# Kernel optimization log

Measured on AMD Instinct MI355X. Metric: run time of the kernel, lower is better.

The kernel has to match this reference:

```python
import jax, jax.numpy as jnp
import numpy as np
import math

B, S, D, DH, R = 2, 2048, 1024, 64, 2


def _hex_grid(radius):
    coords = []
    for q in range(-radius, radius + 1):
        for r in range(max(-radius, -q - radius), min(radius, -q + radius) + 1):
            coords.append((q, r))
    return coords


def _adjacency(coords):
    idx = {c: i for i, c in enumerate(coords)}
    H = len(coords)
    A = np.zeros((H, H), dtype=np.float32)
    dirs = [(1, 0), (1, -1), (0, -1), (-1, 0), (-1, 1), (0, 1)]
    for (q, r), i in idx.items():
        for dq, dr in dirs:
            j = idx.get((q + dq, r + dr))
            if j is not None:
                A[i, j] = 1.0
    return A


def setup_inputs() -> dict:
    key = jax.random.key(0)
    ks = jax.random.split(key, 10)
    coords_list = _hex_grid(R)
    H = len(coords_list)  # 19 heads for radius 2
    coords = jnp.asarray(np.array(coords_list, dtype=np.float32))  # [H,2]
    A = _adjacency(coords_list) + np.eye(H, dtype=np.float32)      # self-loops
    adj_norm = jnp.asarray(A / A.sum(axis=1, keepdims=True))       # row-normalized [H,H]
    sd = 1.0 / math.sqrt(D)
    return {
        "x": jax.random.normal(ks[0], (B, S, D), jnp.float32),
        "coords": coords,
        "w_q": jax.random.normal(ks[1], (H, D, DH), jnp.float32) * sd,
        "w_k": jax.random.normal(ks[2], (H, D, DH), jnp.float32) * sd,
        "w_v": jax.random.normal(ks[3], (H, D, DH), jnp.float32) * sd,
        "wb1": jax.random.normal(ks[4], (2, D), jnp.float32) * 0.5,
        "bb1": jnp.zeros((D,), jnp.float32),
        "wb2": jax.random.normal(ks[5], (D, DH), jnp.float32) * sd,
        "bb2": jnp.zeros((DH,), jnp.float32),
        "w_mix": jax.random.normal(ks[6], (DH, DH), jnp.float32) / math.sqrt(DH),
        "adj_norm": adj_norm,
        "w_o": jax.random.normal(ks[7], (H * DH, D), jnp.float32) * sd,
    }


def reference(x, coords, w_q, w_k, w_v, wb1, bb1, wb2, bb2, w_mix, adj_norm, w_o):
    # coordinate bias: shared MLP mapping hex coord -> d_head bias, added to queries
    bias = jax.nn.relu(coords @ wb1 + bb1) @ wb2 + bb2          # [H,DH]
    # all heads vectorized: q/k/v [B,H,S,DH]
    q = jnp.einsum("bsd,hde->bhse", x, w_q) + bias[None, :, None, :]
    k = jnp.einsum("bsd,hde->bhse", x, w_k)
    v = jnp.einsum("bsd,hde->bhse", x, w_v)
    scores = jnp.einsum("bhse,bhte->bhst", q, k) / math.sqrt(DH)  # [B,H,S,S]
    attn = jax.nn.softmax(scores, axis=-1)
    heads = jnp.einsum("bhst,bhte->bhse", attn, v)               # [B,H,S,DH]
    # GNN mixing over the hex-grid adjacency (residual message passing)
    msg = jax.nn.relu(jnp.einsum("bhse,ef->bhsf", heads, w_mix))
    mixed = heads + jnp.einsum("hg,bgsf->bhsf", adj_norm, msg)   # [B,H,S,DH]
    # concat heads then output projection
    Bx, H, Sx, Dh = mixed.shape
    concat = jnp.transpose(mixed, (0, 2, 1, 3)).reshape(Bx, Sx, H * Dh)
    return concat @ w_o                                          # [B,S,D]
```

## Files before the change

kernel.cpp:

```cpp
#include <hip/hip_runtime.h>
#include <hip/hip_bf16.h>

#define H 19
#define Bv 2
#define Sv 2048
#define Dv 1024
#define DHv 64
#define KK2 (2*H*DHv)
#define QSCALE 0.125f

typedef __bf16 bf16x8 __attribute__((ext_vector_type(8)));
typedef float f32x4 __attribute__((ext_vector_type(4)));

__device__ __forceinline__ ushort f2bf(float f) {
    uint u = __float_as_uint(f);
    u = (u + 0x7fffu + ((u >> 16) & 1u)) >> 16;
    return (ushort)u;
}

__device__ __forceinline__ uint cvtpk(float lo, float hi) {
    uint r;
    asm("v_cvt_pk_bf16_f32 %0, %1, %2" : "=v"(r) : "v"(lo), "v"(hi));
    return r;
}

__device__ __forceinline__ void gll16(const ushort* g, ushort* l) {
    __builtin_amdgcn_global_load_lds(
        (const __attribute__((address_space(1))) unsigned int*)g,
        (__attribute__((address_space(3))) unsigned int*)l, 16, 0, 0);
}

__global__ __launch_bounds__(256) void prep_x(const float* __restrict__ x,
                                              ushort* __restrict__ xbf) {
    int idx = (blockIdx.x*256 + threadIdx.x)*8;
    float4 a = *(const float4*)&x[idx];
    float4 b = *(const float4*)&x[idx+4];
    uint4 o;
    o.x = cvtpk(a.x, a.y);
    o.y = cvtpk(a.z, a.w);
    o.z = cvtpk(b.x, b.y);
    o.w = cvtpk(b.z, b.w);
    *(uint4*)&xbf[idx] = o;
}

__global__ __launch_bounds__(256) void prep_w(const float* __restrict__ wq,
                                              const float* __restrict__ wk,
                                              const float* __restrict__ wv,
                                              ushort* __restrict__ wpackT) {
    const int dt = blockIdx.x, t = blockIdx.y, h = blockIdx.z;
    const float* w = (t == 0) ? wq : (t == 1) ? wk : wv;
    w += (size_t)h*Dv*DHv;
    __shared__ ushort T[64*65];
    const int tid = threadIdx.x;
    int row = tid >> 2, c4 = tid & 3;
    #pragma unroll
    for (int q4 = 0; q4 < 4; ++q4) {
        float4 v = *(const float4*)&w[(size_t)(dt*64+row)*DHv + c4*16 + q4*4];
        T[(c4*16 + q4*4 + 0)*65 + row] = f2bf(v.x);
        T[(c4*16 + q4*4 + 1)*65 + row] = f2bf(v.y);
        T[(c4*16 + q4*4 + 2)*65 + row] = f2bf(v.z);
        T[(c4*16 + q4*4 + 3)*65 + row] = f2bf(v.w);
    }
    __syncthreads();
    #pragma unroll
    for (int i = 0; i < 2; ++i) {
        int f = tid + i*256;
        int e = f >> 3, c = f & 7;
        uint u[4];
        #pragma unroll
        for (int j = 0; j < 4; ++j) {
            uint lo = T[e*65 + c*8 + 2*j];
            uint hi = T[e*65 + c*8 + 2*j + 1];
            u[j] = lo | (hi << 16);
        }
        *(uint4*)&wpackT[((size_t)h*192 + t*64 + e)*Dv + dt*64 + c*8] = make_uint4(u[0],u[1],u[2],u[3]);
    }
}

__global__ __launch_bounds__(256) void prep_wmix(const float* __restrict__ wm,
                                                 ushort* __restrict__ wmixT) {
    int tid = threadIdx.x;
    int e = tid >> 2, f4 = tid & 3;
    #pragma unroll
    for (int j = 0; j < 16; ++j) {
        int f = f4*16 + j;
        wmixT[e*64 + f] = f2bf(wm[f*64 + e]);
    }
}

__global__ __launch_bounds__(256) void prep_wo2(const float* __restrict__ wo,
                                                const float* __restrict__ adj,
                                                ushort* __restrict__ woTcat) {
    const int nt = blockIdx.x;
    const int g  = blockIdx.y;
    const int tid = threadIdx.x;
    const int e = tid >> 2, n4 = tid & 3;
    float acc[16];
    float part1[16];
    #pragma unroll
    for (int j = 0; j < 16; ++j) { acc[j] = 0.f; part1[j] = 0.f; }
    for (int h2 = 0; h2 < H; ++h2) {
        float a = adj[h2*H + g];
        const float* rp = wo + (size_t)(h2*64 + e)*Dv + nt*64 + n4*16;
        #pragma unroll
        for (int j4 = 0; j4 < 4; ++j4) {
            float4 v = *(const float4*)&rp[j4*4];
            acc[j4*4+0] += a*v.x; acc[j4*4+1] += a*v.y;
            acc[j4*4+2] += a*v.z; acc[j4*4+3] += a*v.w;
            if (h2 == g) {
                part1[j4*4+0] = v.x; part1[j4*4+1] = v.y;
                part1[j4*4+2] = v.z; part1[j4*4+3] = v.w;
            }
        }
    }
    #pragma unroll
    for (int j = 0; j < 16; ++j) {
        int n = nt*64 + n4*16 + j;
        woTcat[(size_t)n*KK2 + g*64 + e]            = f2bf(part1[j]);
        woTcat[(size_t)n*KK2 + H*DHv + g*64 + e]    = f2bf(acc[j]);
    }
}

__global__ void bias_kernel(const float* __restrict__ coords,
                            const float* __restrict__ wb1,
                            const float* __restrict__ bb1,
                            const float* __restrict__ wb2,
                            const float* __restrict__ bb2,
                            float* __restrict__ bias) {
    int h = blockIdx.x;
    int e = threadIdx.x;
    float c0 = coords[h*2 + 0];
    float c1 = coords[h*2 + 1];
    float acc = bb2[e];
    for (int d = 0; d < Dv; ++d) {
        float hd = c0*wb1[d] + c1*wb1[Dv + d] + bb1[d];
        hd = fmaxf(hd, 0.0f);
        acc += hd * wb2[d*DHv + e];
    }
    bias[h*DHv + e] = acc;
}

__global__ __launch_bounds__(256) void qkv_mfma(const ushort* __restrict__ xbf,
                                                const ushort* __restrict__ wpackT,
                                                const float* __restrict__ bias,
                                                ushort* __restrict__ qbf,
                                                ushort* __restrict__ kbf,
                                                ushort* __restrict__ vtbf) {
    const int mt = blockIdx.x, h = blockIdx.y;
    const int m0 = mt*64;
    const int tid = threadIdx.x;
    const int w = tid >> 6, lane = tid & 63;
    const int g = lane >> 4, r = lane & 15;

    __shared__ char lds[8192 + 24576];
    char* Xs = lds;
    char* Ws = lds + 8192;
    ushort* VtL = (ushort*)lds;

    f32x4 acc[4][3];
    const f32x4 zf = {0.f,0.f,0.f,0.f};
    #pragma unroll
    for (int m = 0; m < 4; ++m)
        #pragma unroll
        for (int n = 0; n < 3; ++n) acc[m][n] = zf;

    const ushort* xb = xbf + (size_t)m0*Dv;
    const ushort* wb = wpackT + (size_t)h*192*Dv;

    for (int kt = 0; kt < Dv; kt += 64) {
        __syncthreads();
        #pragma unroll
        for (int i = 0; i < 2; ++i) {
            int f = tid + i*256;
            int row = f >> 3, c = f & 7;
            *(bf16x8*)(Xs + row*128 + ((c*16) ^ ((row & 7) << 4))) =
                *(const bf16x8*)(xb + (size_t)row*Dv + kt + c*8);
        }
        #pragma unroll
        for (int i = 0; i < 6; ++i) {
            int f = tid + i*256;
            int row = f >> 3, c = f & 7;
            *(bf16x8*)(Ws + row*128 + ((c*16) ^ ((row & 7) << 4))) =
                *(const bf16x8*)(wb + (size_t)row*Dv + kt + c*8);
        }
        __syncthreads();
        #pragma unroll
        for (int kk = 0; kk < 2; ++kk) {
            bf16x8 a[4], bfr[3];
            #pragma unroll
            for (int m = 0; m < 4; ++m) {
                int row = m*16 + r;
                a[m] = *(const bf16x8*)(Xs + row*128 + (((kk*32 + g*8)*2) ^ ((row & 7) << 4)));
            }
            #pragma unroll
            for (int n = 0; n < 3; ++n) {
                int row = (w*3 + n)*16 + r;
                bfr[n] = *(const bf16x8*)(Ws + row*128 + (((kk*32 + g*8)*2) ^ ((row & 7) << 4)));
            }
            #pragma unroll
            for (int m = 0; m < 4; ++m)
                #pragma unroll
                for (int n = 0; n < 3; ++n)
                    acc[m][n] = __builtin_amdgcn_mfma_f32_16x16x32_bf16(a[m], bfr[n], acc[m][n], 0, 0, 0);
        }
    }

    __syncthreads();

    const int bb = m0 >> 11;
    const int s0 = m0 & 2047;
    #pragma unroll
    for (int m = 0; m < 4; ++m) {
        #pragma unroll
        for (int n = 0; n < 3; ++n) {
            int ng = w*3 + n;
            int t = ng >> 2;
            int e = (ng & 3)*16 + r;
            if (t == 0) {
                float bvv = bias[h*DHv + e];
                #pragma unroll
                for (int reg = 0; reg < 4; ++reg) {
                    int ss = s0 + m*16 + g*4 + reg;
                    qbf[(((size_t)bb*H + h)*Sv + ss)*DHv + e] = f2bf((acc[m][n][reg] + bvv)*QSCALE);
                }
            } else if (t == 1) {
                #pragma unroll
                for (int reg = 0; reg < 4; ++reg) {
                    int ss = s0 + m*16 + g*4 + reg;
                    kbf[(((size_t)bb*H + h)*Sv + ss)*DHv + e] = f2bf(acc[m][n][reg]);
                }
            } else {
                #pragma unroll
                for (int reg = 0; reg < 4; ++reg) {
                    int sl = m*16 + g*4 + reg;
                    VtL[e*66 + sl] = f2bf(acc[m][n][reg]);
                }
            }
        }
    }
    __syncthreads();
    #pragma unroll
    for (int i = 0; i < 2; ++i) {
        int f = tid + i*256;
        int dh = f >> 3, sc = f & 7;
        uint u[4];
        #pragma unroll
        for (int j = 0; j < 4; ++j) {
            uint lo = VtL[dh*66 + sc*8 + 2*j];
            uint hi = VtL[dh*66 + sc*8 + 2*j + 1];
            u[j] = lo | (hi << 16);
        }
        *(uint4*)&vtbf[(((size_t)bb*H + h)*DHv + dh)*Sv + s0 + sc*8] = make_uint4(u[0],u[1],u[2],u[3]);
    }
}

__global__ __launch_bounds__(256) void attn_mfma(const ushort* __restrict__ qg,
                                                 const ushort* __restrict__ kg,
                                                 const ushort* __restrict__ vtg,
                                                 ushort* __restrict__ headsbf) {
    const int qt = blockIdx.x, h = blockIdx.y, b = blockIdx.z;
    const int tid = threadIdx.x;
    const int w = tid >> 6, lane = tid & 63;
    const int g = lane >> 4, r = lane & 15;

    __shared__ ushort Ks[4096];
    __shared__ ushort Vs[4096];
    __shared__ ushort Ps[4][1024];

    const ushort* qb = qg + (((size_t)b*H + h)*Sv + qt*64 + w*16 + r)*DHv;
    const ushort* kb = kg + ((size_t)b*H + h)*Sv*DHv;
    const ushort* vb = vtg + ((size_t)b*H + h)*DHv*Sv;

    bf16x8 qf0 = *(const bf16x8*)(qb + g*8);
    bf16x8 qf1 = *(const bf16x8*)(qb + 32 + g*8);

    float m_run = -1e30f, l_run = 0.f;
    f32x4 o[4];
    const f32x4 zf = {0.f,0.f,0.f,0.f};
    o[0]=zf; o[1]=zf; o[2]=zf; o[3]=zf;

    const int srow = lane >> 3;
    const int scl  = lane & 7;

    for (int jt = 0; jt < Sv/64; ++jt) {
        __syncthreads();
        #pragma unroll
        for (int is = 0; is < 2; ++is) {
            int row = w*16 + is*8 + srow;
            int kcol = (scl ^ (row & 7)) * 8;
            gll16(kb + (size_t)(jt*64 + row)*DHv + kcol, &Ks[(w*16 + is*8)*64]);
            gll16(vb + (size_t)row*Sv + jt*64 + kcol, &Vs[(w*16 + is*8)*64]);
        }
        asm volatile("s_waitcnt vmcnt(0)" ::: "memory");
        __syncthreads();

        f32x4 sc[4];
        sc[0]=zf; sc[1]=zf; sc[2]=zf; sc[3]=zf;
        #pragma unroll
        for (int kk = 0; kk < 2; ++kk) {
            bf16x8 qf = kk ? qf1 : qf0;
            #pragma unroll
            for (int nt = 0; nt < 4; ++nt) {
                int kvrow = nt*16 + r;
                bf16x8 kf = *(const bf16x8*)((const char*)Ks + kvrow*128 +
                                             ((kk*64 + g*16) ^ ((kvrow & 7) << 4)));
                sc[nt] = __builtin_amdgcn_mfma_f32_16x16x32_bf16(kf, qf, sc[nt], 0, 0, 0);
            }
        }

        float pmax = sc[0][0];
        #pragma unroll
        for (int nt = 0; nt < 4; ++nt)
            #pragma unroll
            for (int reg = 0; reg < 4; ++reg)
                pmax = fmaxf(pmax, sc[nt][reg]);
        pmax = fmaxf(pmax, __shfl_xor(pmax, 16));
        pmax = fmaxf(pmax, __shfl_xor(pmax, 32));

        if (__any(pmax > m_run + 8.0f)) {
            float mn = fmaxf(m_run, pmax);
            float corr = __expf(m_run - mn);
            l_run *= corr;
            #pragma unroll
            for (int nt2 = 0; nt2 < 4; ++nt2) {
                o[nt2][0] *= corr; o[nt2][1] *= corr;
                o[nt2][2] *= corr; o[nt2][3] *= corr;
            }
            m_run = mn;
        }

        float lsum = 0.f;
        #pragma unroll
        for (int nt = 0; nt < 4; ++nt) {
            #pragma unroll
            for (int reg = 0; reg < 4; ++reg) {
                float p = __expf(sc[nt][reg] - m_run);
                sc[nt][reg] = p;
                lsum += p;
            }
        }
        lsum += __shfl_xor(lsum, 16);
        lsum += __shfl_xor(lsum, 32);
        l_run += lsum;

        ushort* pw = Ps[w];
        #pragma unroll
        for (int nt = 0; nt < 4; ++nt) {
            uint u0 = cvtpk(sc[nt][0], sc[nt][1]);
            uint u1 = cvtpk(sc[nt][2], sc[nt][3]);
            int chunk = (2*nt + (g >> 1)) ^ (r & 7);
            *(uint2*)((char*)pw + r*128 + (chunk << 4) + ((g & 1)*8)) = make_uint2(u0, u1);
        }

        #pragma unroll
        for (int kk = 0; kk < 2; ++kk) {
            bf16x8 pa = *(const bf16x8*)((const char*)pw + r*128 +
                                         (((kk*4 + g) ^ (r & 7)) << 4));
            #pragma unroll
            for (int nt2 = 0; nt2 < 4; ++nt2) {
                int dh = nt2*16 + r;
                bf16x8 vf = *(const bf16x8*)((const char*)Vs + dh*128 +
                                             ((kk*64 + g*16) ^ ((dh & 7) << 4)));
                o[nt2] = __builtin_amdgcn_mfma_f32_16x16x32_bf16(vf, pa, o[nt2], 0, 0, 0);
            }
        }
    }

    float inv = 1.0f / l_run;
    ushort* hp = headsbf + (((size_t)b*H + h)*Sv + qt*64 + w*16 + r)*DHv;
    #pragma unroll
    for (int nt2 = 0; nt2 < 4; ++nt2) {
        uint u0 = cvtpk(o[nt2][0]*inv, o[nt2][1]*inv);
        uint u1 = cvtpk(o[nt2][2]*inv, o[nt2][3]*inv);
        *(uint2*)(hp + nt2*16 + g*4) = make_uint2(u0, u1);
    }
}

__global__ __launch_bounds__(256) void msg_mfma(const ushort* __restrict__ headsbf,
                                                const ushort* __restrict__ wmixT,
                                                ushort* __restrict__ msgbf) {
    const int st = blockIdx.x, h = blockIdx.y, b = blockIdx.z;
    const int tid = threadIdx.x;
    const int w = tid >> 6, lane = tid & 63;
    const int g = lane >> 4, r = lane & 15;

    __shared__ ushort Hs[4096];
    __shared__ ushort Ws2[4096];

    const ushort* hb = headsbf + ((size_t)((size_t)b*H + h)*Sv + st*64)*DHv;
    const int srow = lane >> 3, scl = lane & 7;
    #pragma unroll
    for (int is = 0; is < 2; ++is) {
        int row = w*16 + is*8 + srow;
        int kcol = (scl ^ (row & 7)) * 8;
        gll16(hb + (size_t)row*DHv + kcol, &Hs[(w*16 + is*8)*64]);
        gll16(wmixT + (size_t)row*DHv + kcol, &Ws2[(w*16 + is*8)*64]);
    }
    asm volatile("s_waitcnt vmcnt(0)" ::: "memory");
    __syncthreads();

    f32x4 acc[4];
    const f32x4 zf = {0.f,0.f,0.f,0.f};
    acc[0]=zf; acc[1]=zf; acc[2]=zf; acc[3]=zf;
    #pragma unroll
    for (int kk = 0; kk < 2; ++kk) {
        int hrow = w*16 + r;
        bf16x8 hf = *(const bf16x8*)((const char*)Hs + hrow*128 +
                                     ((kk*64 + g*16) ^ ((hrow & 7) << 4)));
        #pragma unroll
        for (int nt = 0; nt < 4; ++nt) {
            int erow = nt*16 + r;
            bf16x8 wf = *(const bf16x8*)((const char*)Ws2 + erow*128 +
                                         ((kk*64 + g*16) ^ ((erow & 7) << 4)));
            acc[nt] = __builtin_amdgcn_mfma_f32_16x16x32_bf16(wf, hf, acc[nt], 0, 0, 0);
        }
    }
    ushort* mp = msgbf + ((size_t)((size_t)b*H + h)*Sv + st*64 + w*16 + r)*DHv;
    #pragma unroll
    for (int nt = 0; nt < 4; ++nt) {
        uint u0 = cvtpk(fmaxf(acc[nt][0], 0.f), fmaxf(acc[nt][1], 0.f));
        uint u1 = cvtpk(fmaxf(acc[nt][2], 0.f), fmaxf(acc[nt][3], 0.f));
        *(uint2*)(mp + nt*16 + g*4) = make_uint2(u0, u1);
    }
}

__global__ __launch_bounds__(256) void out_mfma(const ushort* __restrict__ headsbf,
                                                const ushort* __restrict__ msgbf,
                                                const ushort* __restrict__ woTcat,
                                                float* __restrict__ out) {
    const int mt = blockIdx.x, nt2 = blockIdx.y;
    const int m0 = mt*64, n0 = nt2*128;
    const int tid = threadIdx.x;
    const int w = tid >> 6, lane = tid & 63;
    const int g = lane >> 4, r = lane & 15;

    __shared__ char lds[8192 + 16384];
    char* As = lds;
    char* Bs = lds + 8192;

    const int b = m0 >> 11;
    const int s0 = m0 & 2047;

    f32x4 acc[8];
    const f32x4 zf = {0.f,0.f,0.f,0.f};
    #pragma unroll
    for (int n = 0; n < 8; ++n) acc[n] = zf;

    for (int ktile = 0; ktile < KK2/64; ++ktile) {
        const int hh = (ktile < H) ? ktile : ktile - H;
        const ushort* asrc = ((ktile < H) ? headsbf : msgbf) +
                             ((size_t)((size_t)b*H + hh)*Sv + s0)*DHv;
        __syncthreads();
        #pragma unroll
        for (int i = 0; i < 2; ++i) {
            int f = tid + i*256;
            int row = f >> 3, c = f & 7;
            *(bf16x8*)(As + row*128 + ((c*16) ^ ((row & 7) << 4))) =
                *(const bf16x8*)(asrc + (size_t)row*DHv + c*8);
        }
        #pragma unroll
        for (int i = 0; i < 4; ++i) {
            int f = tid + i*256;
            int row = f >> 3, c = f & 7;
            *(bf16x8*)(Bs + row*128 + ((c*16) ^ ((row & 7) << 4))) =
                *(const bf16x8*)(woTcat + (size_t)(n0 + row)*KK2 + ktile*64 + c*8);
        }
        __syncthreads();
        #pragma unroll
        for (int kk = 0; kk < 2; ++kk) {
            int arow = w*16 + r;
            bf16x8 a = *(const bf16x8*)(As + arow*128 + (((kk*32 + g*8)*2) ^ ((arow & 7) << 4)));
            #pragma unroll
            for (int n = 0; n < 8; ++n) {
                int brow = n*16 + r;
                bf16x8 bfr = *(const bf16x8*)(Bs + brow*128 + (((kk*32 + g*8)*2) ^ ((brow & 7) << 4)));
                acc[n] = __builtin_amdgcn_mfma_f32_16x16x32_bf16(a, bfr, acc[n], 0, 0, 0);
            }
        }
    }

    #pragma unroll
    for (int n = 0; n < 8; ++n) {
        #pragma unroll
        for (int reg = 0; reg < 4; ++reg) {
            int grow = m0 + w*16 + g*4 + reg;
            out[(size_t)grow*Dv + n0 + n*16 + r] = acc[n][reg];
        }
    }
}

extern "C" void kernel_launch(void* const* d_in, const int* in_sizes, int n_in,
                              void* d_out, int out_size, void* d_ws, size_t ws_size,
                              hipStream_t stream) {
    const float* x      = (const float*)d_in[0];
    const float* coords = (const float*)d_in[1];
    const float* w_q    = (const float*)d_in[2];
    const float* w_k    = (const float*)d_in[3];
    const float* w_v    = (const float*)d_in[4];
    const float* wb1    = (const float*)d_in[5];
    const float* bb1    = (const float*)d_in[6];
    const float* wb2    = (const float*)d_in[7];
    const float* bb2    = (const float*)d_in[8];
    const float* w_mix  = (const float*)d_in[9];
    const float* adj    = (const float*)d_in[10];
    const float* w_o    = (const float*)d_in[11];

    char* ws = (char*)d_ws;
    const size_t QKV_BYTES = (size_t)Bv*H*Sv*DHv*2;
    const size_t XBF_BYTES = (size_t)Bv*Sv*Dv*2;
    const size_t WPK_BYTES = (size_t)H*192*Dv*2;

    size_t off = 0;
    float*  bias  = (float*)(ws + off);  off += 16384;
    ushort* qbf   = (ushort*)(ws + off); off += QKV_BYTES;
    ushort* kbf   = (ushort*)(ws + off); off += QKV_BYTES;
    ushort* vtbf  = (ushort*)(ws + off); off += QKV_BYTES;
    ushort* hdbf  = (ushort*)(ws + off); off += QKV_BYTES;
    ushort* xbf   = (ushort*)(ws + off);
    ushort* msgbf = xbf;
    off += XBF_BYTES;
    ushort* wpkT  = (ushort*)(ws + off); off += WPK_BYTES;
    ushort* wmixT = (ushort*)(ws + off); off += 8192;
    ushort* woTc  = (ushort*)(ws + off); off += (size_t)Dv*KK2*2;
    float*  out   = (float*)d_out;

    prep_x<<<(Bv*Sv*Dv)/(256*8), 256, 0, stream>>>(x, xbf);
    prep_w<<<dim3(16, 3, H), 256, 0, stream>>>(w_q, w_k, w_v, wpkT);
    prep_wmix<<<1, 256, 0, stream>>>(w_mix, wmixT);
    prep_wo2<<<dim3(16, H), 256, 0, stream>>>(w_o, adj, woTc);
    bias_kernel<<<H, DHv, 0, stream>>>(coords, wb1, bb1, wb2, bb2, bias);
    qkv_mfma<<<dim3(64, H), 256, 0, stream>>>(xbf, wpkT, bias, qbf, kbf, vtbf);
    attn_mfma<<<dim3(Sv/64, H, Bv), 256, 0, stream>>>(qbf, kbf, vtbf, hdbf);
    msg_mfma<<<dim3(Sv/64, H, Bv), 256, 0, stream>>>(hdbf, wmixT, msgbf);
    out_mfma<<<dim3(64, 8), 256, 0, stream>>>(hdbf, msgbf, woTc, out);
}
```

Before: 346.8 us.

## Fuse prep kernels, double-buffer attention K/V, fold msg GEMM into attention

Merges the five preprocessing kernels into a single launch that dispatches on block index, and splits the bias reduction across four waves. The attention kernel now double-buffers K/V tiles so the next tile's global-to-LDS load overlaps the current tile's compute, and uses exp2 with the log2(e) factor folded into the query scale. It also remaps block indices so each XCD handles contiguous heads, and computes the GNN message GEMM in its epilogue, which removes the separate msg kernel and its reload of the heads tensor. The cost is doubled K/V LDS, which may lower occupancy, plus more register pressure from the fused epilogue.

```diff
diff --git a/kernel.cpp b/kernel.cpp
--- a/kernel.cpp
+++ b/kernel.cpp
@@ -7,7 +7,7 @@
 #define Dv 1024
 #define DHv 64
 #define KK2 (2*H*DHv)
-#define QSCALE 0.125f
+#define QSCALE 0.1803368801111204f
 
 typedef __bf16 bf16x8 __attribute__((ext_vector_type(8)));
 typedef float f32x4 __attribute__((ext_vector_type(4)));
@@ -24,120 +24,128 @@
     return r;
 }
 
+__device__ __forceinline__ float fexp2(float x) {
+#if __has_builtin(__builtin_amdgcn_exp2f)
+    return __builtin_amdgcn_exp2f(x);
+#else
+    return exp2f(x);
+#endif
+}
+
 __device__ __forceinline__ void gll16(const ushort* g, ushort* l) {
     __builtin_amdgcn_global_load_lds(
         (const __attribute__((address_space(1))) unsigned int*)g,
         (__attribute__((address_space(3))) unsigned int*)l, 16, 0, 0);
 }
 
-__global__ __launch_bounds__(256) void prep_x(const float* __restrict__ x,
-                                              ushort* __restrict__ xbf) {
-    int idx = (blockIdx.x*256 + threadIdx.x)*8;
-    float4 a = *(const float4*)&x[idx];
-    float4 b = *(const float4*)&x[idx+4];
-    uint4 o;
-    o.x = cvtpk(a.x, a.y);
-    o.y = cvtpk(a.z, a.w);
-    o.z = cvtpk(b.x, b.y);
-    o.w = cvtpk(b.z, b.w);
-    *(uint4*)&xbf[idx] = o;
-}
-
-__global__ __launch_bounds__(256) void prep_w(const float* __restrict__ wq,
-                                              const float* __restrict__ wk,
-                                              const float* __restrict__ wv,
-                                              ushort* __restrict__ wpackT) {
-    const int dt = blockIdx.x, t = blockIdx.y, h = blockIdx.z;
-    const float* w = (t == 0) ? wq : (t == 1) ? wk : wv;
-    w += (size_t)h*Dv*DHv;
-    __shared__ ushort T[64*65];
+#define PX_N 2048
+#define PW_N 912
+#define PWMIX_AT (PX_N + PW_N)
+#define PWO2_AT  (PWMIX_AT + 1)
+#define PBIAS_AT (PWO2_AT + 304)
+#define PREP_N   (PBIAS_AT + H)
+
+__global__ __launch_bounds__(256) void prep_all(
+    const float* __restrict__ x,  const float* __restrict__ wq,
+    const float* __restrict__ wk, const float* __restrict__ wv,
+    const float* __restrict__ wo, const float* __restrict__ adj,
+    const float* __restrict__ wm, const float* __restrict__ coords,
+    const float* __restrict__ wb1, const float* __restrict__ bb1,
+    const float* __restrict__ wb2, const float* __restrict__ bb2,
+    ushort* __restrict__ xbf, ushort* __restrict__ wpackT,
+    ushort* __restrict__ wmixT, ushort* __restrict__ woTcat,
+    float* __restrict__ bias)
+{
+    __shared__ char psm[8448];
+    const int bid = blockIdx.x;
     const int tid = threadIdx.x;
-    int row = tid >> 2, c4 = tid & 3;
-    #pragma unroll
-    for (int q4 = 0; q4 < 4; ++q4) {
-        float4 v = *(const float4*)&w[(size_t)(dt*64+row)*DHv + c4*16 + q4*4];
-        T[(c4*16 + q4*4 + 0)*65 + row] = f2bf(v.x);
-        T[(c4*16 + q4*4 + 1)*65 + row] = f2bf(v.y);
-        T[(c4*16 + q4*4 + 2)*65 + row] = f2bf(v.z);
-        T[(c4*16 + q4*4 + 3)*65 + row] = f2bf(v.w);
-    }
-    __syncthreads();
-    #pragma unroll
-    for (int i = 0; i < 2; ++i) {
-        int f = tid + i*256;
-        int e = f >> 3, c = f & 7;
-        uint u[4];
-        #pragma unroll
-        for (int j = 0; j < 4; ++j) {
-            uint lo = T[e*65 + c*8 + 2*j];
-            uint hi = T[e*65 + c*8 + 2*j + 1];
-            u[j] = lo | (hi << 16);
-        }
-        *(uint4*)&wpackT[((size_t)h*192 + t*64 + e)*Dv + dt*64 + c*8] = make_uint4(u[0],u[1],u[2],u[3]);
-    }
-}
-
-__global__ __launch_bounds__(256) void prep_wmix(const float* __restrict__ wm,
-                                                 ushort* __restrict__ wmixT) {
-    int tid = threadIdx.x;
-    int e = tid >> 2, f4 = tid & 3;
-    #pragma unroll
-    for (int j = 0; j < 16; ++j) {
-        int f = f4*16 + j;
-        wmixT[e*64 + f] = f2bf(wm[f*64 + e]);
-    }
-}
-
-__global__ __launch_bounds__(256) void prep_wo2(const float* __restrict__ wo,
-                                                const float* __restrict__ adj,
-                                                ushort* __restrict__ woTcat) {
-    const int nt = blockIdx.x;
-    const int g  = blockIdx.y;
-    const int tid = threadIdx.x;
-    const int e = tid >> 2, n4 = tid & 3;
-    float acc[16];
-    float part1[16];
-    #pragma unroll
-    for (int j = 0; j < 16; ++j) { acc[j] = 0.f; part1[j] = 0.f; }
-    for (int h2 = 0; h2 < H; ++h2) {
-        float a = adj[h2*H + g];
-        const float* rp = wo + (size_t)(h2*64 + e)*Dv + nt*64 + n4*16;
-        #pragma unroll
-        for (int j4 = 0; j4 < 4; ++j4) {
-            float4 v = *(const float4*)&rp[j4*4];
-            acc[j4*4+0] += a*v.x; acc[j4*4+1] += a*v.y;
-            acc[j4*4+2] += a*v.z; acc[j4*4+3] += a*v.w;
-            if (h2 == g) {
-                part1[j4*4+0] = v.x; part1[j4*4+1] = v.y;
-                part1[j4*4+2] = v.z; part1[j4*4+3] = v.w;
-            }
-        }
-    }
-    #pragma unroll
-    for (int j = 0; j < 16; ++j) {
-        int n = nt*64 + n4*16 + j;
-        woTcat[(size_t)n*KK2 + g*64 + e]            = f2bf(part1[j]);
-        woTcat[(size_t)n*KK2 + H*DHv + g*64 + e]    = f2bf(acc[j]);
-    }
-}
-
-__global__ void bias_kernel(const float* __restrict__ coords,
-                            const float* __restrict__ wb1,
-                            const float* __restrict__ bb1,
-                            const float* __restrict__ wb2,
-                            const float* __restrict__ bb2,
-                            float* __restrict__ bias) {
-    int h = blockIdx.x;
-    int e = threadIdx.x;
-    float c0 = coords[h*2 + 0];
-    float c1 = coords[h*2 + 1];
-    float acc = bb2[e];
-    for (int d = 0; d < Dv; ++d) {
-        float hd = c0*wb1[d] + c1*wb1[Dv + d] + bb1[d];
-        hd = fmaxf(hd, 0.0f);
-        acc += hd * wb2[d*DHv + e];
-    }
-    bias[h*DHv + e] = acc;
+
+    if (bid < PX_N) {
+        int idx = (bid*256 + tid)*8;
+        float4 a = *(const float4*)&x[idx];
+        float4 b = *(const float4*)&x[idx+4];
+        uint4 o;
+        o.x = cvtpk(a.x, a.y); o.y = cvtpk(a.z, a.w);
+        o.z = cvtpk(b.x, b.y); o.w = cvtpk(b.z, b.w);
+        *(uint4*)&xbf[idx] = o;
+    } else if (bid < PWMIX_AT) {
+        ushort* T = (ushort*)psm;
+        int i = bid - PX_N;
+        int dt = i & 15, t = (i >> 4) % 3, h = (i >> 4) / 3;
+        const float* w = (t == 0) ? wq : (t == 1) ? wk : wv;
+        w += (size_t)h*Dv*DHv;
+        int row = tid >> 2, c4 = tid & 3;
+        #pragma unroll
+        for (int q4 = 0; q4 < 4; ++q4) {
+            float4 v = *(const float4*)&w[(size_t)(dt*64+row)*DHv + c4*16 + q4*4];
+            T[(c4*16 + q4*4 + 0)*65 + row] = f2bf(v.x);
+            T[(c4*16 + q4*4 + 1)*65 + row] = f2bf(v.y);
+            T[(c4*16 + q4*4 + 2)*65 + row] = f2bf(v.z);
+            T[(c4*16 + q4*4 + 3)*65 + row] = f2bf(v.w);
+        }
+        __syncthreads();
+        #pragma unroll
+        for (int i2 = 0; i2 < 2; ++i2) {
+            int f = tid + i2*256;
+            int e = f >> 3, c = f & 7;
+            uint u[4];
+            #pragma unroll
+            for (int j = 0; j < 4; ++j) {
+                uint lo = T[e*65 + c*8 + 2*j];
+                uint hi = T[e*65 + c*8 + 2*j + 1];
+                u[j] = lo | (hi << 16);
+            }
+            *(uint4*)&wpackT[((size_t)h*192 + t*64 + e)*Dv + dt*64 + c*8] = make_uint4(u[0],u[1],u[2],u[3]);
+        }
+    } else if (bid == PWMIX_AT) {
+        int e = tid >> 2, f4 = tid & 3;
+        #pragma unroll
+        for (int j = 0; j < 16; ++j) {
+            int f = f4*16 + j;
+            wmixT[e*64 + f] = f2bf(wm[f*64 + e]);
+        }
+    } else if (bid < PBIAS_AT) {
+        int j2 = bid - PWO2_AT;
+        int nt = j2 & 15, g = j2 >> 4;
+        int e = tid >> 2, n4 = tid & 3;
+        float acc[16], part1[16];
+        #pragma unroll
+        for (int j = 0; j < 16; ++j) { acc[j] = 0.f; part1[j] = 0.f; }
+        for (int h2 = 0; h2 < H; ++h2) {
+            float a = adj[h2*H + g];
+            const float* rp = wo + (size_t)(h2*64 + e)*Dv + nt*64 + n4*16;
+            #pragma unroll
+            for (int j4 = 0; j4 < 4; ++j4) {
+                float4 v = *(const float4*)&rp[j4*4];
+                acc[j4*4+0] += a*v.x; acc[j4*4+1] += a*v.y;
+                acc[j4*4+2] += a*v.z; acc[j4*4+3] += a*v.w;
+                if (h2 == g) {
+                    part1[j4*4+0] = v.x; part1[j4*4+1] = v.y;
+                    part1[j4*4+2] = v.z; part1[j4*4+3] = v.w;
+                }
+            }
+        }
+        #pragma unroll
+        for (int j = 0; j < 16; ++j) {
+            int n = nt*64 + n4*16 + j;
+            woTcat[(size_t)n*KK2 + g*64 + e]         = f2bf(part1[j]);
+            woTcat[(size_t)n*KK2 + H*DHv + g*64 + e] = f2bf(acc[j]);
+        }
+    } else {
+        float* part = (float*)psm;
+        int hh = bid - PBIAS_AT;
+        int e = tid & 63, quar = tid >> 6;
+        float c0 = coords[hh*2], c1 = coords[hh*2+1];
+        float acc = (quar == 0) ? bb2[e] : 0.f;
+        int d0 = quar*256;
+        for (int d = d0; d < d0+256; ++d) {
+            float t2 = fmaxf(c0*wb1[d] + c1*wb1[Dv+d] + bb1[d], 0.f);
+            acc += t2 * wb2[d*DHv + e];
+        }
+        if (quar) part[(quar-1)*64 + e] = acc;
+        __syncthreads();
+        if (quar == 0) bias[hh*DHv + e] = acc + part[e] + part[64+e] + part[128+e];
+    }
 }
 
 __global__ __launch_bounds__(256) void qkv_mfma(const ushort* __restrict__ xbf,
@@ -257,19 +265,28 @@
 __global__ __launch_bounds__(256) void attn_mfma(const ushort* __restrict__ qg,
                                                  const ushort* __restrict__ kg,
                                                  const ushort* __restrict__ vtg,
-                                                 ushort* __restrict__ headsbf) {
-    const int qt = blockIdx.x, h = blockIdx.y, b = blockIdx.z;
+                                                 const ushort* __restrict__ wmixT,
+                                                 ushort* __restrict__ headsbf,
+                                                 ushort* __restrict__ msgbf) {
+    const int hw = blockIdx.x;
+    const int logical = (hw & 7) * 152 + (hw >> 3);
+    const int qt = logical & 31;
+    const int hb = logical >> 5;
+    const int h = hb % H, b = hb / H;
+
     const int tid = threadIdx.x;
     const int w = tid >> 6, lane = tid & 63;
     const int g = lane >> 4, r = lane & 15;
-
-    __shared__ ushort Ks[4096];
-    __shared__ ushort Vs[4096];
+    const int srow = lane >> 3, scl = lane & 7;
+
+    __shared__ ushort Ks[2][4096];
+    __shared__ ushort Vs[2][4096];
     __shared__ ushort Ps[4][1024];
 
-    const ushort* qb = qg + (((size_t)b*H + h)*Sv + qt*64 + w*16 + r)*DHv;
-    const ushort* kb = kg + ((size_t)b*H + h)*Sv*DHv;
-    const ushort* vb = vtg + ((size_t)b*H + h)*DHv*Sv;
+    const size_t bh = (size_t)b*H + h;
+    const ushort* kb = kg + bh*Sv*DHv;
+    const ushort* vb = vtg + bh*DHv*Sv;
+    const ushort* qb = qg + (bh*Sv + qt*64 + w*16 + r)*DHv;
 
     bf16x8 qf0 = *(const bf16x8*)(qb + g*8);
     bf16x8 qf1 = *(const bf16x8*)(qb + 32 + g*8);
@@ -279,20 +296,32 @@
     const f32x4 zf = {0.f,0.f,0.f,0.f};
     o[0]=zf; o[1]=zf; o[2]=zf; o[3]=zf;
 
-    const int srow = lane >> 3;
-    const int scl  = lane & 7;
-
-    for (int jt = 0; jt < Sv/64; ++jt) {
-        __syncthreads();
+    auto STAGE = [&](int jt_, int bi_) {
         #pragma unroll
         for (int is = 0; is < 2; ++is) {
             int row = w*16 + is*8 + srow;
             int kcol = (scl ^ (row & 7)) * 8;
-            gll16(kb + (size_t)(jt*64 + row)*DHv + kcol, &Ks[(w*16 + is*8)*64]);
-            gll16(vb + (size_t)row*Sv + jt*64 + kcol, &Vs[(w*16 + is*8)*64]);
-        }
-        asm volatile("s_waitcnt vmcnt(0)" ::: "memory");
-        __syncthreads();
+            gll16(kb + (size_t)(jt_*64 + row)*DHv + kcol, &Ks[bi_][(w*16 + is*8)*64]);
+            gll16(vb + (size_t)row*Sv + jt_*64 + kcol, &Vs[bi_][(w*16 + is*8)*64]);
+        }
+    };
+
+    STAGE(0, 0);
+
+    for (int jt = 0; jt < Sv/64; ++jt) {
+        const int cur = jt & 1;
+        if (jt < Sv/64 - 1) {
+            STAGE(jt+1, cur^1);
+            asm volatile("s_waitcnt vmcnt(4)" ::: "memory");
+        } else {
+            asm volatile("s_waitcnt vmcnt(0)" ::: "memory");
+        }
+        __builtin_amdgcn_sched_barrier(0);
+        __builtin_amdgcn_s_barrier();
+        __builtin_amdgcn_sched_barrier(0);
+
+        const ushort* Kc = Ks[cur];
+        const ushort* Vc = Vs[cur];
 
         f32x4 sc[4];
         sc[0]=zf; sc[1]=zf; sc[2]=zf; sc[3]=zf;
@@ -302,7 +331,7 @@
             #pragma unroll
             for (int nt = 0; nt < 4; ++nt) {
                 int kvrow = nt*16 + r;
-                bf16x8 kf = *(const bf16x8*)((const char*)Ks + kvrow*128 +
+                bf16x8 kf = *(const bf16x8*)((const char*)Kc + kvrow*128 +
                                              ((kk*64 + g*16) ^ ((kvrow & 7) << 4)));
                 sc[nt] = __builtin_amdgcn_mfma_f32_16x16x32_bf16(kf, qf, sc[nt], 0, 0, 0);
             }
@@ -319,7 +348,7 @@
 
         if (__any(pmax > m_run + 8.0f)) {
             float mn = fmaxf(m_run, pmax);
-            float corr = __expf(m_run - mn);
+            float corr = fexp2(m_run - mn);
             l_run *= corr;
             #pragma unroll
             for (int nt2 = 0; nt2 < 4; ++nt2) {
@@ -334,7 +363,7 @@
         for (int nt = 0; nt < 4; ++nt) {
             #pragma unroll
             for (int reg = 0; reg < 4; ++reg) {
-                float p = __expf(sc[nt][reg] - m_run);
+                float p = fexp2(sc[nt][reg] - m_run);
                 sc[nt][reg] = p;
                 lsum += p;
             }
@@ -359,67 +388,49 @@
             #pragma unroll
             for (int nt2 = 0; nt2 < 4; ++nt2) {
                 int dh = nt2*16 + r;
-                bf16x8 vf = *(const bf16x8*)((const char*)Vs + dh*128 +
+                bf16x8 vf = *(const bf16x8*)((const char*)Vc + dh*128 +
                                              ((kk*64 + g*16) ^ ((dh & 7) << 4)));
                 o[nt2] = __builtin_amdgcn_mfma_f32_16x16x32_bf16(vf, pa, o[nt2], 0, 0, 0);
             }
         }
+        __builtin_amdgcn_sched_barrier(0);
+        __builtin_amdgcn_s_barrier();
     }
 
     float inv = 1.0f / l_run;
-    ushort* hp = headsbf + (((size_t)b*H + h)*Sv + qt*64 + w*16 + r)*DHv;
+    ushort* hp = headsbf + (bh*Sv + qt*64 + w*16 + r)*DHv;
+    ushort* pw = Ps[w];
     #pragma unroll
     for (int nt2 = 0; nt2 < 4; ++nt2) {
         uint u0 = cvtpk(o[nt2][0]*inv, o[nt2][1]*inv);
         uint u1 = cvtpk(o[nt2][2]*inv, o[nt2][3]*inv);
         *(uint2*)(hp + nt2*16 + g*4) = make_uint2(u0, u1);
-    }
-}
-
-__global__ __launch_bounds__(256) void msg_mfma(const ushort* __restrict__ headsbf,
-                                                const ushort* __restrict__ wmixT,
-                                                ushort* __restrict__ msgbf) {
-    const int st = blockIdx.x, h = blockIdx.y, b = blockIdx.z;
-    const int tid = threadIdx.x;
-    const int w = tid >> 6, lane = tid & 63;
-    const int g = lane >> 4, r = lane & 15;
-
-    __shared__ ushort Hs[4096];
-    __shared__ ushort Ws2[4096];
-
-    const ushort* hb = headsbf + ((size_t)((size_t)b*H + h)*Sv + st*64)*DHv;
-    const int srow = lane >> 3, scl = lane & 7;
-    #pragma unroll
-    for (int is = 0; is < 2; ++is) {
-        int row = w*16 + is*8 + srow;
-        int kcol = (scl ^ (row & 7)) * 8;
-        gll16(hb + (size_t)row*DHv + kcol, &Hs[(w*16 + is*8)*64]);
-        gll16(wmixT + (size_t)row*DHv + kcol, &Ws2[(w*16 + is*8)*64]);
-    }
-    asm volatile("s_waitcnt vmcnt(0)" ::: "memory");
-    __syncthreads();
-
-    f32x4 acc[4];
-    const f32x4 zf = {0.f,0.f,0.f,0.f};
-    acc[0]=zf; acc[1]=zf; acc[2]=zf; acc[3]=zf;
+        int chunk = (2*nt2 + (g >> 1)) ^ (r & 7);
+        *(uint2*)((char*)pw + r*128 + (chunk << 4) + ((g & 1)*8)) = make_uint2(u0, u1);
+    }
+
+    bf16x8 wmf[2][4];
+    #pragma unroll
+    for (int kk = 0; kk < 2; ++kk)
+        #pragma unroll
+        for (int nt = 0; nt < 4; ++nt)
+            wmf[kk][nt] = *(const bf16x8*)(wmixT + (nt*16 + r)*64 + kk*32 + g*8);
+
+    f32x4 macc[4];
+    macc[0]=zf; macc[1]=zf; macc[2]=zf; macc[3]=zf;
     #pragma unroll
     for (int kk = 0; kk < 2; ++kk) {
-        int hrow = w*16 + r;
-        bf16x8 hf = *(const bf16x8*)((const char*)Hs + hrow*128 +
-                                     ((kk*64 + g*16) ^ ((hrow & 7) << 4)));
-        #pragma unroll
-        for (int nt = 0; nt < 4; ++nt) {
-            int erow = nt*16 + r;
-            bf16x8 wf = *(const bf16x8*)((const char*)Ws2 + erow*128 +
-                                         ((kk*64 + g*16) ^ ((erow & 7) << 4)));
-            acc[nt] = __builtin_amdgcn_mfma_f32_16x16x32_bf16(wf, hf, acc[nt], 0, 0, 0);
-        }
-    }
-    ushort* mp = msgbf + ((size_t)((size_t)b*H + h)*Sv + st*64 + w*16 + r)*DHv;
+        bf16x8 pa = *(const bf16x8*)((const char*)pw + r*128 +
+                                     (((kk*4 + g) ^ (r & 7)) << 4));
+        #pragma unroll
+        for (int nt = 0; nt < 4; ++nt)
+            macc[nt] = __builtin_amdgcn_mfma_f32_16x16x32_bf16(wmf[kk][nt], pa, macc[nt], 0, 0, 0);
+    }
+    ushort* mp = msgbf + (bh*Sv + qt*64 + w*16 + r)*DHv;
     #pragma unroll
     for (int nt = 0; nt < 4; ++nt) {
-        uint u0 = cvtpk(fmaxf(acc[nt][0], 0.f), fmaxf(acc[nt][1], 0.f));
-        uint u1 = cvtpk(fmaxf(acc[nt][2], 0.f), fmaxf(acc[nt][3], 0.f));
+        uint u0 = cvtpk(fmaxf(macc[nt][0], 0.f), fmaxf(macc[nt][1], 0.f));
+        uint u1 = cvtpk(fmaxf(macc[nt][2], 0.f), fmaxf(macc[nt][3], 0.f));
         *(uint2*)(mp + nt*16 + g*4) = make_uint2(u0, u1);
     }
 }
@@ -524,13 +535,10 @@
     ushort* woTc  = (ushort*)(ws + off); off += (size_t)Dv*KK2*2;
     float*  out   = (float*)d_out;
 
-    prep_x<<<(Bv*Sv*Dv)/(256*8), 256, 0, stream>>>(x, xbf);
-    prep_w<<<dim3(16, 3, H), 256, 0, stream>>>(w_q, w_k, w_v, wpkT);
-    prep_wmix<<<1, 256, 0, stream>>>(w_mix, wmixT);
-    prep_wo2<<<dim3(16, H), 256, 0, stream>>>(w_o, adj, woTc);
-    bias_kernel<<<H, DHv, 0, stream>>>(coords, wb1, bb1, wb2, bb2, bias);
+    prep_all<<<PREP_N, 256, 0, stream>>>(x, w_q, w_k, w_v, w_o, adj, w_mix,
+                                         coords, wb1, bb1, wb2, bb2,
+                                         xbf, wpkT, wmixT, woTc, bias);
     qkv_mfma<<<dim3(64, H), 256, 0, stream>>>(xbf, wpkT, bias, qbf, kbf, vtbf);
-    attn_mfma<<<dim3(Sv/64, H, Bv), 256, 0, stream>>>(qbf, kbf, vtbf, hdbf);
-    msg_mfma<<<dim3(Sv/64, H, Bv), 256, 0, stream>>>(hdbf, wmixT, msgbf);
+    attn_mfma<<<1216, 256, 0, stream>>>(qbf, kbf, vtbf, wmixT, hdbf, msgbf);
     out_mfma<<<dim3(64, 8), 256, 0, stream>>>(hdbf, msgbf, woTc, out);
 }
```

Result: slower. 356.9 us (+2.9%).
